# Kernel optimization log

Measured on AMD Instinct MI355X. Metric: run time of the kernel, lower is better.

The kernel has to match this reference:

```python
import jax, jax.numpy as jnp
import numpy as np

GRID_BOUND = 0.5
GRID_SIZE = 64


def _reflect(points, p):
    # points: [B, N, 3], p: [B, 4] plane (a, b, c, d) -> reflect about ax+by+cz+d=0
    n = p[:, :3]                                   # [B, 3]
    d = p[:, 3]                                    # [B]
    denom = jnp.sum(n * n, axis=-1) + 1e-12        # [B]
    t = (jnp.einsum('bnc,bc->bn', points, n) + d[:, None]) / denom[:, None]  # [B, N]
    return points - 2.0 * t[..., None] * n[:, None, :]


def _rotate(points, q):
    # points: [B, N, 3], q: [B, 4] quaternion (w, x, y, z), normalized here
    q = q / (jnp.linalg.norm(q, axis=-1, keepdims=True) + 1e-12)
    w = q[:, 0][:, None, None]                     # [B, 1, 1]
    v = q[:, 1:][:, None, :]                       # [B, 1, 3]
    uv = jnp.cross(v, points)                      # [B, N, 3]
    return points + 2.0 * jnp.cross(v, uv + w * points)


def _cal_distance(pts, cp):
    # pts: [B, N, 3]; cp: [B, G^3, 3] nearest-surface-point per voxel cell
    gs = GRID_SIZE
    # map [-gridBound, gridBound] -> voxel index in [0, gs-1]
    idx = jnp.clip(jnp.floor((pts / (2.0 * GRID_BOUND) + 0.5) * gs), 0, gs - 1).astype(jnp.int32)
    flat = (idx[..., 0] * gs + idx[..., 1]) * gs + idx[..., 2]   # [B, N]
    nearest = jnp.take_along_axis(cp, flat[..., None], axis=1)   # [B, N, 3] irregular gather
    return jnp.mean(jnp.sum((pts - nearest) ** 2, axis=-1))


def setup_inputs() -> dict:
    key = jax.random.key(0)
    k1, k2, k3, k4, k5 = jax.random.split(key, 5)
    B, N, K, gs = 128, 8192, 3, GRID_SIZE
    points = jax.random.uniform(k1, (B, N, 3), jnp.float32) - 0.5   # in [-0.5, 0.5]
    cp = jax.random.uniform(k2, (B, gs ** 3, 3), jnp.float32) - 0.5
    voxel = jax.random.uniform(k3, (B, gs, gs, gs), jnp.float32)
    plane = jax.random.normal(k4, (K, B, 4), jnp.float32)
    quat = jax.random.normal(k5, (K, B, 4), jnp.float32)
    return {"points": points, "cp": cp, "voxel": voxel, "plane": plane, "quat": quat}


def reference(points, cp, voxel, plane, quat):
    # voxel is carried for API fidelity (used only by the custom backward in the
    # original CUDA op); forward math depends on points/cp/plane/quat.
    del voxel
    # vectorize across all K symmetries instead of the original Python loop
    ref_pts = jax.vmap(_reflect, in_axes=(None, 0))(points, plane)  # [K, B, N, 3]
    rot_pts = jax.vmap(_rotate, in_axes=(None, 0))(points, quat)    # [K, B, N, 3]
    ref_loss = jnp.sum(jax.vmap(_cal_distance, in_axes=(0, None))(ref_pts, cp))
    rot_loss = jnp.sum(jax.vmap(_cal_distance, in_axes=(0, None))(rot_pts, cp))
    return ref_loss, rot_loss
```

## Files before the change

### kernel.cpp

```cpp
#include <hip/hip_runtime.h>

#define GS 64
#define BB 128
#define NN 8192
#define KK 3
#define SLICE_FLOATS (GS * GS * GS * 3)
#define B_PER_XCD 16
#define BLOCKS_PER_B 96
#define GRID (BB * BLOCKS_PER_B)
#define SEQ_PER_XCD (GRID / 8)

__global__ __launch_bounds__(256) void symloss_main(
    const float* __restrict__ points, const float* __restrict__ cp,
    const float* __restrict__ plane, const float* __restrict__ quat,
    float2* __restrict__ partials) {
    int raw = blockIdx.x;
    int xcd = raw & 7;
    int s   = raw >> 3;
    int b   = xcd * B_PER_XCD + s / BLOCKS_PER_B;
    int j   = s % BLOCKS_PER_B;
    int k   = j % 3;
    int chunk = j / 3;
    int n = chunk * 256 + threadIdx.x;

    const float* p = points + ((size_t)b * NN + n) * 3;
    float px = p[0], py = p[1], pz = p[2];
    const float* cpb = cp + (size_t)b * SLICE_FLOATS;

    const float* plk = plane + ((size_t)k * BB + b) * 4;
    float nx = plk[0], ny = plk[1], nz = plk[2], d = plk[3];
    float denom = nx * nx + ny * ny + nz * nz + 1e-12f;
    float tt = (px * nx + py * ny + pz * nz + d) / denom;
    float rx = px - 2.0f * tt * nx;
    float ry = py - 2.0f * tt * ny;
    float rz = pz - 2.0f * tt * nz;

    const float* q = quat + ((size_t)k * BB + b) * 4;
    float qw = q[0], qx = q[1], qy = q[2], qz = q[3];
    float qn = sqrtf(qw * qw + qx * qx + qy * qy + qz * qz) + 1e-12f;
    qw /= qn; qx /= qn; qy /= qn; qz /= qn;
    float ux = qy * pz - qz * py;
    float uy = qz * px - qx * pz;
    float uz = qx * py - qy * px;
    float sx = ux + qw * px;
    float sy = uy + qw * py;
    float sz = uz + qw * pz;
    float ox = px + 2.0f * (qy * sz - qz * sy);
    float oy = py + 2.0f * (qz * sx - qx * sz);
    float oz = pz + 2.0f * (qx * sy - qy * sx);

    float fx = fminf(fmaxf(floorf((rx + 0.5f) * 64.0f), 0.0f), 63.0f);
    float fy = fminf(fmaxf(floorf((ry + 0.5f) * 64.0f), 0.0f), 63.0f);
    float fz = fminf(fmaxf(floorf((rz + 0.5f) * 64.0f), 0.0f), 63.0f);
    int flat_r = (((int)fx * GS) + (int)fy) * GS + (int)fz;
    float gx = fminf(fmaxf(floorf((ox + 0.5f) * 64.0f), 0.0f), 63.0f);
    float gy = fminf(fmaxf(floorf((oy + 0.5f) * 64.0f), 0.0f), 63.0f);
    float gz = fminf(fmaxf(floorf((oz + 0.5f) * 64.0f), 0.0f), 63.0f);
    int flat_o = (((int)gx * GS) + (int)gy) * GS + (int)gz;

    const float* cr = cpb + (size_t)flat_r * 3;
    const float* co = cpb + (size_t)flat_o * 3;
    float c0 = cr[0], c1 = cr[1], c2 = cr[2];
    float e0 = co[0], e1 = co[1], e2 = co[2];

    float drx = rx - c0, dry = ry - c1, drz = rz - c2;
    float dox = ox - e0, doy = oy - e1, doz = oz - e2;
    float ref_acc = drx * drx + dry * dry + drz * drz;
    float rot_acc = dox * dox + doy * doy + doz * doz;

    for (int off = 32; off > 0; off >>= 1) {
        ref_acc += __shfl_down(ref_acc, off, 64);
        rot_acc += __shfl_down(rot_acc, off, 64);
    }
    __shared__ float s_ref[4], s_rot[4];
    int wave = threadIdx.x >> 6;
    int lane = threadIdx.x & 63;
    if (lane == 0) {
        s_ref[wave] = ref_acc;
        s_rot[wave] = rot_acc;
    }
    __syncthreads();
    if (threadIdx.x == 0) {
        float2 v;
        v.x = s_ref[0] + s_ref[1] + s_ref[2] + s_ref[3];
        v.y = s_rot[0] + s_rot[1] + s_rot[2] + s_rot[3];
        partials[blockIdx.x] = v;
    }
}

__global__ __launch_bounds__(1024) void finalize_kernel(
    const float2* __restrict__ partials, float* __restrict__ out) {
    double r = 0.0, o = 0.0;
    for (int i = threadIdx.x; i < GRID; i += 1024) {
        float2 v = partials[i];
        r += (double)v.x;
        o += (double)v.y;
    }
    __shared__ double s_r[1024], s_o[1024];
    s_r[threadIdx.x] = r;
    s_o[threadIdx.x] = o;
    __syncthreads();
    for (int off = 512; off > 0; off >>= 1) {
        if (threadIdx.x < off) {
            s_r[threadIdx.x] += s_r[threadIdx.x + off];
            s_o[threadIdx.x] += s_o[threadIdx.x + off];
        }
        __syncthreads();
    }
    if (threadIdx.x == 0) {
        const double inv = 1.0 / ((double)BB * (double)NN);
        out[0] = (float)(s_r[0] * inv);
        out[1] = (float)(s_o[0] * inv);
    }
}

extern "C" void kernel_launch(void* const* d_in, const int* in_sizes, int n_in,
                              void* d_out, int out_size, void* d_ws, size_t ws_size,
                              hipStream_t stream) {
    const float* points = (const float*)d_in[0];
    const float* cp     = (const float*)d_in[1];
    const float* plane  = (const float*)d_in[3];
    const float* quat   = (const float*)d_in[4];
    float* out = (float*)d_out;
    float2* partials = (float2*)d_ws;

    symloss_main<<<GRID, 256, 0, stream>>>(points, cp, plane, quat, partials);
    finalize_kernel<<<1, 1024, 0, stream>>>(partials, out);
}
```

Before: 65.29 us.

## Pad main kernel LDS to cap occupancy and slim finalize reduction

Launches the main kernel with 48KB of unused dynamic shared memory, which limits how many blocks can be resident per CU. The likely intent is to cut cache thrashing from the random gathers into cp. The finalize kernel now uses 256 threads, float4 loads and wave shuffles in place of a 1024-wide LDS tree. Capping occupancy reduces the latency hiding available to the gather-bound main kernel.

```diff
diff --git a/kernel.cpp b/kernel.cpp
--- a/kernel.cpp
+++ b/kernel.cpp
@@ -8,12 +8,14 @@
 #define B_PER_XCD 16
 #define BLOCKS_PER_B 96
 #define GRID (BB * BLOCKS_PER_B)
-#define SEQ_PER_XCD (GRID / 8)
+#define LDS_PAD 49152
 
 __global__ __launch_bounds__(256) void symloss_main(
     const float* __restrict__ points, const float* __restrict__ cp,
     const float* __restrict__ plane, const float* __restrict__ quat,
     float2* __restrict__ partials) {
+    extern __shared__ char lds_pad[];
+
     int raw = blockIdx.x;
     int xcd = raw & 7;
     int s   = raw >> 3;
@@ -88,29 +90,30 @@
     }
 }
 
-__global__ __launch_bounds__(1024) void finalize_kernel(
-    const float2* __restrict__ partials, float* __restrict__ out) {
+__global__ __launch_bounds__(256) void finalize_kernel(
+    const float4* __restrict__ partials4, float* __restrict__ out) {
     double r = 0.0, o = 0.0;
-    for (int i = threadIdx.x; i < GRID; i += 1024) {
-        float2 v = partials[i];
-        r += (double)v.x;
-        o += (double)v.y;
+    for (int i = threadIdx.x; i < GRID / 2; i += 256) {
+        float4 v = partials4[i];
+        r += (double)v.x + (double)v.z;
+        o += (double)v.y + (double)v.w;
     }
-    __shared__ double s_r[1024], s_o[1024];
-    s_r[threadIdx.x] = r;
-    s_o[threadIdx.x] = o;
+    for (int off = 32; off > 0; off >>= 1) {
+        r += __shfl_down(r, off, 64);
+        o += __shfl_down(o, off, 64);
+    }
+    __shared__ double s_r[4], s_o[4];
+    int wave = threadIdx.x >> 6;
+    int lane = threadIdx.x & 63;
+    if (lane == 0) {
+        s_r[wave] = r;
+        s_o[wave] = o;
+    }
     __syncthreads();
-    for (int off = 512; off > 0; off >>= 1) {
-        if (threadIdx.x < off) {
-            s_r[threadIdx.x] += s_r[threadIdx.x + off];
-            s_o[threadIdx.x] += s_o[threadIdx.x + off];
-        }
-        __syncthreads();
-    }
     if (threadIdx.x == 0) {
         const double inv = 1.0 / ((double)BB * (double)NN);
-        out[0] = (float)(s_r[0] * inv);
-        out[1] = (float)(s_o[0] * inv);
+        out[0] = (float)((s_r[0] + s_r[1] + s_r[2] + s_r[3]) * inv);
+        out[1] = (float)((s_o[0] + s_o[1] + s_o[2] + s_o[3]) * inv);
     }
 }
 
@@ -124,6 +127,7 @@
     float* out = (float*)d_out;
     float2* partials = (float2*)d_ws;
 
-    symloss_main<<<GRID, 256, 0, stream>>>(points, cp, plane, quat, partials);
-    finalize_kernel<<<1, 1024, 0, stream>>>(partials, out);
+    symloss_main<<<GRID, 256, LDS_PAD, stream>>>(points, cp, plane, quat,
+                                                 partials);
+    finalize_kernel<<<1, 256, 0, stream>>>((const float4*)partials, out);
 }
```

Result: slower. 81.08 us (+24.2%).
